# Kernel optimization log

Hardware: AMD Instinct MI355X
Metric: run time of the kernel (lower is better)

Reference implementation:

```python
import jax, jax.numpy as jnp
import numpy as np

B, T, N = 2, 256, 512
H, S, C = 64, 8, 8
DYN = 4


def setup_inputs() -> dict:
    key = jax.random.key(0)
    ks = jax.random.split(key, 12)
    sc = 0.05
    return {
        "x": jax.random.normal(ks[0], (B, T, N), jnp.float32),
        "mask": (jax.random.uniform(ks[1], (B, T, N)) < 0.2).astype(jnp.float32),
        "static_context": jax.random.normal(ks[2], (N, S), jnp.float32),
        "node_coords": jax.random.normal(ks[3], (N, C), jnp.float32),
        "W1": jax.random.normal(ks[4], (DYN + S, H), jnp.float32) * sc,
        "b1": jnp.zeros((H,), jnp.float32),
        "W2": jax.random.normal(ks[5], (H, H), jnp.float32) * sc,
        "b2": jnp.zeros((H,), jnp.float32),
        "We1": jax.random.normal(ks[6], (4 * H, H), jnp.float32) * sc,
        "be1": jnp.zeros((H,), jnp.float32),
        "We2": jax.random.normal(ks[7], (H, 1), jnp.float32) * sc,
        "be2": jnp.zeros((1,), jnp.float32),
        "self_loop_logit": jnp.float32(0.5),
        "prior_strength": jnp.float32(1.0),
        "similarity_strength": jnp.float32(1.0),
        "temperature": jnp.float32(0.7),
    }


def reference(x, mask, static_context, node_coords, W1, b1, W2, b2,
              We1, be1, We2, be2, self_loop_logit, prior_strength,
              similarity_strength, temperature):
    Bv, Tv, Nv = x.shape
    # ---- dynamic per-node context over time ----
    observed = 1.0 - mask                                   # [B,T,N]
    count = jnp.maximum(observed.sum(axis=1), 1.0)          # [B,N]
    mean = (x * observed).sum(axis=1) / count               # [B,N]
    centered = (x - mean[:, None, :]) * observed
    std = jnp.sqrt((centered ** 2).sum(axis=1) / count + 1e-6)
    t_idx = jnp.arange(Tv, dtype=x.dtype)[None, :, None]
    latest = jnp.argmax(t_idx * observed, axis=1)           # [B,N] int
    last = jnp.take_along_axis(x, latest[:, None, :], axis=1)[:, 0, :]
    missing_ratio = mask.mean(axis=1)
    dyn = jnp.stack([mean, std, last, missing_ratio], axis=-1)  # [B,N,4]
    # ---- node encoder ----
    static = jnp.broadcast_to(static_context[None], (Bv, Nv, static_context.shape[-1]))
    feats = jnp.concatenate([dyn, static], axis=-1)
    h = jax.nn.relu(feats @ W1 + b1)
    h = jax.nn.relu(h @ W2 + b2)                            # [B,N,H]
    hn = h / jnp.maximum(jnp.linalg.norm(h, axis=-1, keepdims=True), 1e-12)
    # ---- edge MLP on pair features [h_i, h_j, |h_i-h_j|, h_i*h_j] ----
    # split first-layer weight into the four blocks so h_i/h_j terms are O(N)
    Wi, Wj, Wa, Wp = jnp.split(We1, 4, axis=0)              # each [H,H]
    pre_i = h @ Wi                                          # [B,N,H]
    pre_j = h @ Wj
    hi = h[:, :, None, :]                                   # [B,N,1,H]
    hj = h[:, None, :, :]                                   # [B,1,N,H]
    hidden = jax.nn.relu(pre_i[:, :, None, :] + pre_j[:, None, :, :]
                         + jnp.abs(hi - hj) @ Wa + (hi * hj) @ Wp + be1)
    edge_logits = (hidden @ We2 + be2)[..., 0]              # [B,N,N]
    # ---- cosine similarity + distance prior ----
    cos = jnp.einsum('bnh,bmh->bnm', hn, hn)
    eye = jnp.eye(Nv, dtype=x.dtype)
    off = 1.0 - eye
    diff = node_coords[:, None, :] - node_coords[None, :, :]
    dist = jnp.sqrt(jnp.maximum((diff ** 2).sum(-1), 1e-12))
    prior = (1.0 / (1.0 + dist)) * off                      # [N,N]
    # ---- combine, softmax, symmetrize, row-normalize ----
    logits = (edge_logits * off
              + jax.nn.softplus(prior_strength) * prior[None]
              + jax.nn.softplus(similarity_strength) * (cos * off))
    logits = logits + eye[None] * jax.nn.softplus(self_loop_logit)
    temp = jax.nn.softplus(temperature) + 1e-4
    adj = jax.nn.softmax(logits / temp, axis=-1)
    adj = 0.5 * (adj + jnp.swapaxes(adj, -1, -2))
    adj = adj / jnp.maximum(adj.sum(axis=-1, keepdims=True), 1e-6)
    return adj
```

## Files before the change

kernel.cpp:

```cpp
#include <hip/hip_runtime.h>
#include <hip/hip_bf16.h>
#include <math.h>

#define NB 2
#define NT 256
#define NN 512
#define NH 64
#define NS 8
#define NC 8

#define OFF_H      0
#define OFF_PVEC   65536
#define OFF_HF16   131072
#define OFF_INVN   163840
#define OFF_WA16   164864
#define OFF_WJF    166912
#define OFF_WPF    171008
#define OFF_UNSYM  175104
#define OFF_UNSYMT (175104 + 524288)

typedef __attribute__((ext_vector_type(8))) _Float16 h8;
typedef __attribute__((ext_vector_type(2))) __fp16 fp16x2;
typedef __attribute__((ext_vector_type(4))) float f32x4;
typedef __attribute__((ext_vector_type(4))) unsigned u4;
typedef __attribute__((ext_vector_type(2))) unsigned u2;

__device__ __forceinline__ float softplusf(float x){
  if (x > 20.f) return x;
  return log1pf(expf(x));
}

__device__ __forceinline__ unsigned pkh(float a, float b){
  fp16x2 h = __builtin_amdgcn_cvt_pkrtz(a, b);
  return __builtin_bit_cast(unsigned, h);
}

__device__ __forceinline__ float fdot2u(unsigned a, unsigned b, float c){
#if __has_builtin(__builtin_amdgcn_fdot2)
  return __builtin_amdgcn_fdot2(__builtin_bit_cast(fp16x2, a),
                                __builtin_bit_cast(fp16x2, b), c, false);
#else
  fp16x2 av = __builtin_bit_cast(fp16x2, a);
  fp16x2 bv = __builtin_bit_cast(fp16x2, b);
  return fmaf((float)av.x, (float)bv.x, fmaf((float)av.y, (float)bv.y, c));
#endif
}
__device__ __forceinline__ float dot8(u4 a, u4 b, float acc){
  #pragma unroll
  for (int d = 0; d < 4; ++d) acc = fdot2u(a[d], b[d], acc);
  return acc;
}

template<int CTRL>
__device__ __forceinline__ float dpp_addf(float x){
  int xi = __builtin_bit_cast(int, x);
  int yi = __builtin_amdgcn_update_dpp(0, xi, CTRL, 0xF, 0xF, true);
  return x + __builtin_bit_cast(float, yi);
}
__device__ __forceinline__ float row16_sum(float x){
  x = dpp_addf<0xB1>(x);
  x = dpp_addf<0x4E>(x);
  x = dpp_addf<0x141>(x);
  x = dpp_addf<0x140>(x);
  return x;
}

__global__ __launch_bounds__(256) void k_front(
    const float* __restrict__ x, const float* __restrict__ mask,
    const float* __restrict__ sctx,
    const float* __restrict__ W1, const float* __restrict__ b1,
    const float* __restrict__ W2, const float* __restrict__ b2,
    const float* __restrict__ We1, const float* __restrict__ be1,
    float* __restrict__ hg, float* __restrict__ pvec,
    unsigned* __restrict__ hf16, float* __restrict__ invn,
    short* __restrict__ wa16, float* __restrict__ wjf,
    float* __restrict__ wpf){
  int blk = blockIdx.x;
  int tid = threadIdx.x;

  if (blk >= 256){
    int pidx = (blk - 256)*256 + tid;
    int e    = pidx & 7;
    int lane = (pidx >> 3) & 63;
    int frag = (pidx >> 9) & 7;
    int nt = frag & 3, ks = frag >> 2;
    int kg = lane >> 4, q = lane & 15;
    int kk = ks*32 + kg*8 + e;
    int c  = nt*16 + q;
    if (pidx < 4096){
      _Float16 v = (_Float16)We1[(128 + kk)*NH + c];
      wa16[pidx] = __builtin_bit_cast(short, v);
    } else if (pidx < 8192){
      wjf[pidx - 4096] = We1[(64 + kk)*NH + c];
    } else {
      wpf[pidx - 8192] = We1[(192 + kk)*NH + c];
    }
    return;
  }

  int b  = blk >> 7;
  int n0 = (blk & 127) * 4;

  int nl = tid & 3;
  int ts = tid >> 2;
  int n  = n0 + nl;

  float cnt = 0.f, sx = 0.f, sxx = 0.f;
  int lastt = 0;
  for (int t = ts*4; t < ts*4 + 4; ++t){
    int idx = (b*NT + t)*NN + n;
    float xv = x[idx];
    float mv = mask[idx];
    bool obs = (mv < 0.5f);
    if (obs){ cnt += 1.f; sx += xv; sxx += xv*xv; lastt = t; }
  }
  #pragma unroll
  for (int m = 4; m < 64; m <<= 1){
    cnt   += __shfl_xor(cnt,  m);
    sx    += __shfl_xor(sx,   m);
    sxx   += __shfl_xor(sxx,  m);
    lastt  = max(lastt, __shfl_xor(lastt, m));
  }
  int w = tid >> 6;
  __shared__ float r_cnt[4][4], r_sx[4][4], r_sxx[4][4];
  __shared__ int   r_lt[4][4];
  __shared__ float s_dyn[4][4];
  if ((tid & 63) < 4){
    r_cnt[w][nl] = cnt; r_sx[w][nl] = sx; r_sxx[w][nl] = sxx; r_lt[w][nl] = lastt;
  }
  __syncthreads();
  if (tid < 4){
    float c = 0.f, s1 = 0.f, s2 = 0.f; int lt = 0;
    #pragma unroll
    for (int ww = 0; ww < 4; ++ww){
      c  += r_cnt[ww][tid]; s1 += r_sx[ww][tid]; s2 += r_sxx[ww][tid];
      lt  = max(lt, r_lt[ww][tid]);
    }
    float cc   = fmaxf(c, 1.f);
    float mean = s1 / cc;
    float var  = s2 / cc - mean*mean;
    float stdv = sqrtf(fmaxf(var, 0.f) + 1e-6f);
    float last = x[(b*NT + lt)*NN + n0 + tid];
    float mr   = 1.f - c * (1.f/(float)NT);
    s_dyn[tid][0] = mean; s_dyn[tid][1] = stdv; s_dyn[tid][2] = last; s_dyn[tid][3] = mr;
  }
  __syncthreads();

  int c = tid & 63;
  int gn = n0 + w;
  int bn = b*NN + gn;
  __shared__ float s_f[4][12];
  __shared__ float s_h1[4][64];
  __shared__ float s_h2[4][64];

  if (c < 4)       s_f[w][c] = s_dyn[w][c];
  else if (c < 12) s_f[w][c] = sctx[gn*NS + (c-4)];
  __syncthreads();

  float a = b1[c];
  #pragma unroll
  for (int k = 0; k < 12; ++k) a = fmaf(s_f[w][k], W1[k*NH + c], a);
  s_h1[w][c] = fmaxf(a, 0.f);
  __syncthreads();

  float t0 = 0.f, t1 = 0.f, t2 = 0.f, t3 = 0.f;
  #pragma unroll 4
  for (int k = 0; k < 64; k += 4){
    t0 = fmaf(s_h1[w][k],     W2[(k)*NH + c],     t0);
    t1 = fmaf(s_h1[w][k + 1], W2[(k + 1)*NH + c], t1);
    t2 = fmaf(s_h1[w][k + 2], W2[(k + 2)*NH + c], t2);
    t3 = fmaf(s_h1[w][k + 3], W2[(k + 3)*NH + c], t3);
  }
  float a2 = b2[c] + ((t0 + t1) + (t2 + t3));
  a2 = fmaxf(a2, 0.f);

  float sq = a2*a2;
  #pragma unroll
  for (int m = 1; m < 64; m <<= 1) sq += __shfl_xor(sq, m);
  float inv = 1.f / fmaxf(sqrtf(sq), 1e-12f);

  s_h2[w][c] = a2;
  __syncthreads();

  float p0 = 0.f, p1 = 0.f, p2 = 0.f, p3 = 0.f;
  #pragma unroll 4
  for (int k = 0; k < 64; k += 4){
    p0 = fmaf(s_h2[w][k],     We1[(k)*NH + c],     p0);
    p1 = fmaf(s_h2[w][k + 1], We1[(k + 1)*NH + c], p1);
    p2 = fmaf(s_h2[w][k + 2], We1[(k + 2)*NH + c], p2);
    p3 = fmaf(s_h2[w][k + 3], We1[(k + 3)*NH + c], p3);
  }
  float pi = be1[c] + ((p0 + p1) + (p2 + p3));

  hg  [bn*64 + c] = a2;
  pvec[bn*64 + c] = pi;
  if (c < 32){
    float e0 = s_h2[w][2*c], e1 = s_h2[w][2*c + 1];
    hf16[bn*32 + c] = pkh(e0, e1);
  }
  if (c == 0) invn[bn] = inv;
}

__global__ __launch_bounds__(512, 4) void k_logits(
    const float* __restrict__ hg, const float* __restrict__ pvec,
    const unsigned* __restrict__ hf16, const float* __restrict__ invn,
    const short* __restrict__ wa16, const float* __restrict__ wjf,
    const float* __restrict__ wpf, const float* __restrict__ coords,
    const float* __restrict__ We2, const float* __restrict__ be2,
    const float* __restrict__ s_sl, const float* __restrict__ s_ps,
    const float* __restrict__ s_ss, const float* __restrict__ s_tp,
    float* __restrict__ unsym, float* __restrict__ unsymT){
  int blk = blockIdx.x;
  int b  = blk >> 8;
  int ip = (blk & 255) * 2;
  int tid  = threadIdx.x;
  int w    = tid >> 6;
  int lane = tid & 63;
  int q    = lane & 15;
  int kg   = lane >> 4;

  __shared__ __align__(16) float s_hi[2][64];
  __shared__ __align__(16) float s_pri[2][NN];
  __shared__ __align__(16) float s_invn[NN];
  __shared__ __align__(16) float lrow[2][NN];
  __shared__ __align__(16) unsigned lds_wa[2048];
  __shared__ __align__(16) unsigned lds_cw[2][2048];
  __shared__ __align__(16) unsigned s_hj[8][2][16*34 + 2];
  __shared__ float red[32];

  float spsl = softplusf(s_sl[0]);
  float spps = softplusf(s_ps[0]);
  float spss = softplusf(s_ss[0]);
  float invt = 1.f / (softplusf(s_tp[0]) + 1e-4f);
  float be2v = be2[0];

  if (tid < 128)
    s_hi[tid >> 6][tid & 63] = hg[(b*NN + ip + (tid >> 6))*64 + (tid & 63)];
  {
    int j = tid;
    float4 cj0 = *(const float4*)(coords + j*NC);
    float4 cj1 = *(const float4*)(coords + j*NC + 4);
    #pragma unroll
    for (int r = 0; r < 2; ++r){
      int i = ip + r;
      float4 ci0 = *(const float4*)(coords + i*NC);
      float4 ci1 = *(const float4*)(coords + i*NC + 4);
      float dd = 0.f;
      dd = fmaf(ci0.x-cj0.x, ci0.x-cj0.x, dd);
      dd = fmaf(ci0.y-cj0.y, ci0.y-cj0.y, dd);
      dd = fmaf(ci0.z-cj0.z, ci0.z-cj0.z, dd);
      dd = fmaf(ci0.w-cj0.w, ci0.w-cj0.w, dd);
      dd = fmaf(ci1.x-cj1.x, ci1.x-cj1.x, dd);
      dd = fmaf(ci1.y-cj1.y, ci1.y-cj1.y, dd);
      dd = fmaf(ci1.z-cj1.z, ci1.z-cj1.z, dd);
      dd = fmaf(ci1.w-cj1.w, ci1.w-cj1.w, dd);
      float dist = sqrtf(fmaxf(dd, 1e-12f));
      s_pri[r][j] = (j == i) ? be2v : fmaf(spps, 1.f/(1.f + dist), be2v);
    }
    s_invn[j] = invn[b*NN + j];
  }
  __syncthreads();

  {
    int frag = tid >> 6;
    int l2   = tid & 63;
    const u4* wsrc = (const u4*)wa16;
    *(u4*)&lds_wa[(frag*64 + l2)*4] = wsrc[frag*64 + l2];

    int ch0 = (frag >> 2)*32 + (l2 >> 4)*8;
    const float* wj = wjf + (frag*64 + l2)*8;
    const float* wp = wpf + (frag*64 + l2)*8;
    #pragma unroll
    for (int r = 0; r < 2; ++r){
      u4 u;
      #pragma unroll
      for (int d = 0; d < 4; ++d){
        float v0 = fmaf(s_hi[r][ch0 + 2*d],     wp[2*d],     wj[2*d]);
        float v1 = fmaf(s_hi[r][ch0 + 2*d + 1], wp[2*d + 1], wj[2*d + 1]);
        u[d] = pkh(v0, v1);
      }
      *(u4*)&lds_cw[r][(frag*64 + l2)*4] = u;
    }
  }

  const u4* hfv = (const u4*)hf16;
  u4 hiA[2][2];
  #pragma unroll
  for (int r = 0; r < 2; ++r){
    hiA[r][0] = hfv[(b*NN + ip + r)*8 + kg];
    hiA[r][1] = hfv[(b*NN + ip + r)*8 + kg + 4];
  }

  float pv4[2][4], we2q[4];
  #pragma unroll
  for (int nt = 0; nt < 4; ++nt){
    #pragma unroll
    for (int r = 0; r < 2; ++r)
      pv4[r][nt] = pvec[(b*NN + ip + r)*64 + nt*16 + q];
    we2q[nt] = We2[nt*16 + q];
  }
  float invni[2];
  invni[0] = invn[b*NN + ip];
  invni[1] = invn[b*NN + ip + 1];
  int srcl = (lane & 48) | (((lane >> 4) & 3) << 2) | (lane & 3);
  int r8 = lane >> 3, c8 = lane & 7;
  __syncthreads();

  const u4 absm = (u4){0x7fff7fffu, 0x7fff7fffu, 0x7fff7fffu, 0x7fff7fffu};

  u4 g0, g1;
  {
    int jbase = w * 16;
    g0 = *(const u4*)((const unsigned*)hf16 + (size_t)(b*NN + jbase + r8)*32 + c8*4);
    g1 = *(const u4*)((const unsigned*)hf16 + (size_t)(b*NN + jbase + 8 + r8)*32 + c8*4);
  }

  #pragma unroll
  for (int s = 0; s < 4; ++s){
    int jbase = (w + s*8) * 16;
    unsigned* slice = &s_hj[w][s & 1][0];

    {
      unsigned* p0 = slice + r8*34 + c8*4;
      unsigned* p1 = slice + (8 + r8)*34 + c8*4;
      u2 t;
      t.x = g0.x; t.y = g0.y; *(u2*)p0 = t;
      t.x = g0.z; t.y = g0.w; *(u2*)(p0 + 2) = t;
      t.x = g1.x; t.y = g1.y; *(u2*)p1 = t;
      t.x = g1.z; t.y = g1.w; *(u2*)(p1 + 2) = t;
    }
    if (s < 3){
      int jn = (w + (s+1)*8) * 16;
      g0 = *(const u4*)((const unsigned*)hf16 + (size_t)(b*NN + jn + r8)*32 + c8*4);
      g1 = *(const u4*)((const unsigned*)hf16 + (size_t)(b*NN + jn + 8 + r8)*32 + c8*4);
    }

    u4 hj0, hj1;
    {
      unsigned* rp = slice + q*34 + kg*4;
      u2 a0 = *(u2*)rp;
      u2 a1 = *(u2*)(rp + 2);
      u2 b0 = *(u2*)(rp + 16);
      u2 b1 = *(u2*)(rp + 18);
      hj0.x = a0.x; hj0.y = a0.y; hj0.z = a1.x; hj0.w = a1.y;
      hj1.x = b0.x; hj1.y = b0.y; hj1.z = b1.x; hj1.w = b1.y;
    }
    h8 hjv0 = __builtin_bit_cast(h8, hj0);
    h8 hjv1 = __builtin_bit_cast(h8, hj1);

    float dotp[2];
    #pragma unroll
    for (int r = 0; r < 2; ++r){
      float d0 = dot8(hiA[r][0], hj0, 0.f);
      dotp[r]  = dot8(hiA[r][1], hj1, d0);
    }

    f32x4 acc[2][4];
    #pragma unroll
    for (int r = 0; r < 2; ++r)
      #pragma unroll
      for (int nt = 0; nt < 4; ++nt)
        acc[r][nt] = (f32x4){pv4[r][nt], pv4[r][nt], pv4[r][nt], pv4[r][nt]};

    #pragma unroll
    for (int nt = 0; nt < 4; ++nt){
      h8 wA0 = __builtin_bit_cast(h8, *(const u4*)&lds_wa[((0*4 + nt)*64 + lane)*4]);
      h8 wA1 = __builtin_bit_cast(h8, *(const u4*)&lds_wa[((1*4 + nt)*64 + lane)*4]);
      #pragma unroll
      for (int r = 0; r < 2; ++r){
        h8 dh0 = __builtin_bit_cast(h8, hiA[r][0]) - hjv0;
        h8 dh1 = __builtin_bit_cast(h8, hiA[r][1]) - hjv1;
        h8 af0 = __builtin_bit_cast(h8, __builtin_bit_cast(u4, dh0) & absm);
        h8 af1 = __builtin_bit_cast(h8, __builtin_bit_cast(u4, dh1) & absm);
        h8 wC0 = __builtin_bit_cast(h8, *(const u4*)&lds_cw[r][((0*4 + nt)*64 + lane)*4]);
        h8 wC1 = __builtin_bit_cast(h8, *(const u4*)&lds_cw[r][((1*4 + nt)*64 + lane)*4]);
        acc[r][nt] = __builtin_amdgcn_mfma_f32_16x16x32_f16(af0, wA0, acc[r][nt], 0, 0, 0);
        acc[r][nt] = __builtin_amdgcn_mfma_f32_16x16x32_f16(af1, wA1, acc[r][nt], 0, 0, 0);
        acc[r][nt] = __builtin_amdgcn_mfma_f32_16x16x32_f16(hjv0, wC0, acc[r][nt], 0, 0, 0);
        acc[r][nt] = __builtin_amdgcn_mfma_f32_16x16x32_f16(hjv1, wC1, acc[r][nt], 0, 0, 0);
      }
    }

    #pragma unroll
    for (int r = 0; r < 2; ++r){
      float part[4] = {0.f, 0.f, 0.f, 0.f};
      #pragma unroll
      for (int nt = 0; nt < 4; ++nt)
        #pragma unroll
        for (int rr = 0; rr < 4; ++rr)
          part[rr] = fmaf(fmaxf(acc[r][nt][rr], 0.f), we2q[nt], part[rr]);
      #pragma unroll
      for (int rr = 0; rr < 4; ++rr) part[rr] = row16_sum(part[rr]);

      float dp = dotp[r];
      dp += __shfl_xor(dp, 16);
      dp += __shfl_xor(dp, 32);
      float dj = __shfl(dp, srcl);

      if (q < 4){
        int j2 = jbase + kg*4 + q;
        float ps2 = part[0];
        ps2 = (q == 1) ? part[1] : ps2;
        ps2 = (q == 2) ? part[2] : ps2;
        ps2 = (q == 3) ? part[3] : ps2;
        float cosv = dj * invni[r] * s_invn[j2];
        lrow[r][j2] = ps2 + s_pri[r][j2] + spss * cosv;
      }
    }
  }
  __syncthreads();

  float va = (tid == ip)     ? spsl : lrow[0][tid];
  float vb = (tid == ip + 1) ? spsl : lrow[1][tid];

  float ma = va, mb = vb;
  #pragma unroll
  for (int msk = 1; msk < 64; msk <<= 1){
    ma = fmaxf(ma, __shfl_xor(ma, msk));
    mb = fmaxf(mb, __shfl_xor(mb, msk));
  }
  if (lane == 0){ red[w] = ma; red[8 + w] = mb; }
  __syncthreads();
  ma = red[0]; mb = red[8];
  #pragma unroll
  for (int ww = 1; ww < 8; ++ww){
    ma = fmaxf(ma, red[ww]);
    mb = fmaxf(mb, red[8 + ww]);
  }

  float ea = expf((va - ma) * invt);
  float eb = expf((vb - mb) * invt);
  float sa = ea, sb = eb;
  #pragma unroll
  for (int msk = 1; msk < 64; msk <<= 1){
    sa += __shfl_xor(sa, msk);
    sb += __shfl_xor(sb, msk);
  }
  if (lane == 0){ red[16 + w] = sa; red[24 + w] = sb; }
  __syncthreads();
  sa = red[16]; sb = red[24];
  #pragma unroll
  for (int ww = 1; ww < 8; ++ww){
    sa += red[16 + ww];
    sb += red[24 + ww];
  }

  float oa = ea / sa;
  float ob = eb / sb;
  unsym[(size_t)(b*NN + ip)*NN + tid]     = oa;
  unsym[(size_t)(b*NN + ip + 1)*NN + tid] = ob;
  *(float2*)(unsymT + (size_t)(b*NN + tid)*NN + ip) = (float2){oa, ob};
}

__global__ __launch_bounds__(512) void k_sym(
    const float* __restrict__ u, const float* __restrict__ ut,
    float* __restrict__ out){
  int blk = blockIdx.x;
  int b  = blk >> 8;
  int ip = (blk & 255) * 2;
  int tid  = threadIdx.x;
  int lane = tid & 63, w = tid >> 6;

  const float* ra  = u  + (size_t)(b*NN + ip) * NN;
  const float* rat = ut + (size_t)(b*NN + ip) * NN;
  const float* rb  = u  + (size_t)(b*NN + ip + 1) * NN;
  const float* rbt = ut + (size_t)(b*NN + ip + 1) * NN;
  float va = 0.5f*(ra[tid] + rat[tid]);
  float vb = 0.5f*(rb[tid] + rbt[tid]);

  float sa = va, sb = vb;
  #pragma unroll
  for (int msk = 1; msk < 64; msk <<= 1){
    sa += __shfl_xor(sa, msk);
    sb += __shfl_xor(sb, msk);
  }
  __shared__ float red[16];
  if (lane == 0){ red[w] = sa; red[8 + w] = sb; }
  __syncthreads();
  sa = red[0]; sb = red[8];
  #pragma unroll
  for (int ww = 1; ww < 8; ++ww){
    sa += red[ww];
    sb += red[8 + ww];
  }
  float ia = 1.f / fmaxf(sa, 1e-6f);
  float ib = 1.f / fmaxf(sb, 1e-6f);
  out[(size_t)(b*NN + ip)*NN + tid]     = va * ia;
  out[(size_t)(b*NN + ip + 1)*NN + tid] = vb * ib;
}

extern "C" void kernel_launch(void* const* d_in, const int* in_sizes, int n_in,
                              void* d_out, int out_size, void* d_ws, size_t ws_size,
                              hipStream_t stream){
  const float* x      = (const float*)d_in[0];
  const float* mask   = (const float*)d_in[1];
  const float* sctx   = (const float*)d_in[2];
  const float* coords = (const float*)d_in[3];
  const float* W1     = (const float*)d_in[4];
  const float* b1     = (const float*)d_in[5];
  const float* W2     = (const float*)d_in[6];
  const float* b2     = (const float*)d_in[7];
  const float* We1    = (const float*)d_in[8];
  const float* be1    = (const float*)d_in[9];
  const float* We2    = (const float*)d_in[10];
  const float* be2    = (const float*)d_in[11];
  const float* sl     = (const float*)d_in[12];
  const float* ps     = (const float*)d_in[13];
  const float* ss     = (const float*)d_in[14];
  const float* tp     = (const float*)d_in[15];

  float*    ws     = (float*)d_ws;
  float*    hgp    = ws + OFF_H;
  float*    pvecp  = ws + OFF_PVEC;
  unsigned* hf16p  = (unsigned*)(ws + OFF_HF16);
  float*    invnp  = ws + OFF_INVN;
  short*    wa16p  = (short*)(ws + OFF_WA16);
  float*    wjfp   = ws + OFF_WJF;
  float*    wpfp   = ws + OFF_WPF;
  float*    unsym  = ws + OFF_UNSYM;
  float*    unsymT = ws + OFF_UNSYMT;
  float*    out    = (float*)d_out;

  k_front <<<304, 256, 0, stream>>>(x, mask, sctx, W1, b1, W2, b2, We1, be1,
                                    hgp, pvecp, hf16p, invnp, wa16p, wjfp, wpfp);
  k_logits<<<NB*NN/2, 512, 0, stream>>>(hgp, pvecp, hf16p, invnp, wa16p, wjfp,
                                        wpfp, coords, We2, be2, sl, ps, ss, tp,
                                        unsym, unsymT);
  k_sym   <<<NB*NN/2, 512, 0, stream>>>(unsym, unsymT, out);
}
```

Baseline: 39.93 us.

## Process four rows per block in k_logits with 1024-thread blocks

Each k_logits block now handles four i-rows instead of two, using 1024 threads and 16 waves. Each wave covers two 16-column j-tiles and loops over two row pairs, so one staged h_j tile and the shared lds_wa weights serve twice as many rows. The softmax is split so each half of the block reduces its own pair of rows. This halves the grid to 256 blocks and raises LDS per block, which may lower occupancy and leave fewer blocks to spread across CUs.

```diff
diff --git a/kernel.cpp b/kernel.cpp
--- a/kernel.cpp
+++ b/kernel.cpp
@@ -201,7 +201,7 @@
   if (c == 0) invn[bn] = inv;
 }
 
-__global__ __launch_bounds__(512, 4) void k_logits(
+__global__ __launch_bounds__(1024, 4) void k_logits(
     const float* __restrict__ hg, const float* __restrict__ pvec,
     const unsigned* __restrict__ hf16, const float* __restrict__ invn,
     const short* __restrict__ wa16, const float* __restrict__ wjf,
@@ -211,22 +211,24 @@
     const float* __restrict__ s_ss, const float* __restrict__ s_tp,
     float* __restrict__ unsym, float* __restrict__ unsymT){
   int blk = blockIdx.x;
-  int b  = blk >> 8;
-  int ip = (blk & 255) * 2;
+  int b  = blk >> 7;
+  int ip = (blk & 127) * 4;
   int tid  = threadIdx.x;
   int w    = tid >> 6;
   int lane = tid & 63;
   int q    = lane & 15;
   int kg   = lane >> 4;
-
-  __shared__ __align__(16) float s_hi[2][64];
-  __shared__ __align__(16) float s_pri[2][NN];
+  int half = tid >> 9;
+  int jj   = tid & 511;
+
+  __shared__ __align__(16) float s_hi[4][64];
+  __shared__ __align__(16) float s_pri[4][NN];
   __shared__ __align__(16) float s_invn[NN];
-  __shared__ __align__(16) float lrow[2][NN];
+  __shared__ __align__(16) float lrow[4][NN];
   __shared__ __align__(16) unsigned lds_wa[2048];
-  __shared__ __align__(16) unsigned lds_cw[2][2048];
-  __shared__ __align__(16) unsigned s_hj[8][2][16*34 + 2];
-  __shared__ float red[32];
+  __shared__ __align__(16) unsigned lds_cw[4][2048];
+  __shared__ __align__(16) unsigned s_hj[16][16*34 + 2];
+  __shared__ float red[64];
 
   float spsl = softplusf(s_sl[0]);
   float spps = softplusf(s_ps[0]);
@@ -234,15 +236,16 @@
   float invt = 1.f / (softplusf(s_tp[0]) + 1e-4f);
   float be2v = be2[0];
 
-  if (tid < 128)
+  if (tid < 256)
     s_hi[tid >> 6][tid & 63] = hg[(b*NN + ip + (tid >> 6))*64 + (tid & 63)];
   {
-    int j = tid;
+    int j = jj;
     float4 cj0 = *(const float4*)(coords + j*NC);
     float4 cj1 = *(const float4*)(coords + j*NC + 4);
     #pragma unroll
     for (int r = 0; r < 2; ++r){
-      int i = ip + r;
+      int row = half*2 + r;
+      int i = ip + row;
       float4 ci0 = *(const float4*)(coords + i*NC);
       float4 ci1 = *(const float4*)(coords + i*NC + 4);
       float dd = 0.f;
@@ -255,58 +258,53 @@
       dd = fmaf(ci1.z-cj1.z, ci1.z-cj1.z, dd);
       dd = fmaf(ci1.w-cj1.w, ci1.w-cj1.w, dd);
       float dist = sqrtf(fmaxf(dd, 1e-12f));
-      s_pri[r][j] = (j == i) ? be2v : fmaf(spps, 1.f/(1.f + dist), be2v);
-    }
-    s_invn[j] = invn[b*NN + j];
+      s_pri[row][j] = (j == i) ? be2v : fmaf(spps, 1.f/(1.f + dist), be2v);
+    }
+    if (half == 0) s_invn[j] = invn[b*NN + j];
   }
   __syncthreads();
 
   {
-    int frag = tid >> 6;
+    int frag = (tid >> 6) & 7;
     int l2   = tid & 63;
-    const u4* wsrc = (const u4*)wa16;
-    *(u4*)&lds_wa[(frag*64 + l2)*4] = wsrc[frag*64 + l2];
+    if (half == 0)
+      *(u4*)&lds_wa[(frag*64 + l2)*4] = ((const u4*)wa16)[frag*64 + l2];
 
     int ch0 = (frag >> 2)*32 + (l2 >> 4)*8;
     const float* wj = wjf + (frag*64 + l2)*8;
     const float* wp = wpf + (frag*64 + l2)*8;
     #pragma unroll
     for (int r = 0; r < 2; ++r){
+      int row = half*2 + r;
       u4 u;
       #pragma unroll
       for (int d = 0; d < 4; ++d){
-        float v0 = fmaf(s_hi[r][ch0 + 2*d],     wp[2*d],     wj[2*d]);
-        float v1 = fmaf(s_hi[r][ch0 + 2*d + 1], wp[2*d + 1], wj[2*d + 1]);
+        float v0 = fmaf(s_hi[row][ch0 + 2*d],     wp[2*d],     wj[2*d]);
+        float v1 = fmaf(s_hi[row][ch0 + 2*d + 1], wp[2*d + 1], wj[2*d + 1]);
         u[d] = pkh(v0, v1);
       }
-      *(u4*)&lds_cw[r][(frag*64 + l2)*4] = u;
+      *(u4*)&lds_cw[row][(frag*64 + l2)*4] = u;
     }
   }
 
   const u4* hfv = (const u4*)hf16;
-  u4 hiA[2][2];
-  #pragma unroll
-  for (int r = 0; r < 2; ++r){
-    hiA[r][0] = hfv[(b*NN + ip + r)*8 + kg];
-    hiA[r][1] = hfv[(b*NN + ip + r)*8 + kg + 4];
-  }
-
-  float pv4[2][4], we2q[4];
+  float pv4[4][4], we2q[4];
   #pragma unroll
   for (int nt = 0; nt < 4; ++nt){
     #pragma unroll
-    for (int r = 0; r < 2; ++r)
-      pv4[r][nt] = pvec[(b*NN + ip + r)*64 + nt*16 + q];
+    for (int row = 0; row < 4; ++row)
+      pv4[row][nt] = pvec[(b*NN + ip + row)*64 + nt*16 + q];
     we2q[nt] = We2[nt*16 + q];
   }
-  float invni[2];
-  invni[0] = invn[b*NN + ip];
-  invni[1] = invn[b*NN + ip + 1];
+  float invni[4];
+  #pragma unroll
+  for (int row = 0; row < 4; ++row) invni[row] = invn[b*NN + ip + row];
   int srcl = (lane & 48) | (((lane >> 4) & 3) << 2) | (lane & 3);
   int r8 = lane >> 3, c8 = lane & 7;
   __syncthreads();
 
   const u4 absm = (u4){0x7fff7fffu, 0x7fff7fffu, 0x7fff7fffu, 0x7fff7fffu};
+  unsigned* slice = &s_hj[w][0];
 
   u4 g0, g1;
   {
@@ -316,9 +314,8 @@
   }
 
   #pragma unroll
-  for (int s = 0; s < 4; ++s){
-    int jbase = (w + s*8) * 16;
-    unsigned* slice = &s_hj[w][s & 1][0];
+  for (int s = 0; s < 2; ++s){
+    int jbase = (w + s*16) * 16;
 
     {
       unsigned* p0 = slice + r8*34 + c8*4;
@@ -329,8 +326,8 @@
       t.x = g1.x; t.y = g1.y; *(u2*)p1 = t;
       t.x = g1.z; t.y = g1.w; *(u2*)(p1 + 2) = t;
     }
-    if (s < 3){
-      int jn = (w + (s+1)*8) * 16;
+    if (s == 0){
+      int jn = (w + 16) * 16;
       g0 = *(const u4*)((const unsigned*)hf16 + (size_t)(b*NN + jn + r8)*32 + c8*4);
       g1 = *(const u4*)((const unsigned*)hf16 + (size_t)(b*NN + jn + 8 + r8)*32 + c8*4);
     }
@@ -348,108 +345,126 @@
     h8 hjv0 = __builtin_bit_cast(h8, hj0);
     h8 hjv1 = __builtin_bit_cast(h8, hj1);
 
-    float dotp[2];
-    #pragma unroll
-    for (int r = 0; r < 2; ++r){
-      float d0 = dot8(hiA[r][0], hj0, 0.f);
-      dotp[r]  = dot8(hiA[r][1], hj1, d0);
-    }
-
-    f32x4 acc[2][4];
-    #pragma unroll
-    for (int r = 0; r < 2; ++r)
-      #pragma unroll
-      for (int nt = 0; nt < 4; ++nt)
-        acc[r][nt] = (f32x4){pv4[r][nt], pv4[r][nt], pv4[r][nt], pv4[r][nt]};
-
-    #pragma unroll
-    for (int nt = 0; nt < 4; ++nt){
-      h8 wA0 = __builtin_bit_cast(h8, *(const u4*)&lds_wa[((0*4 + nt)*64 + lane)*4]);
-      h8 wA1 = __builtin_bit_cast(h8, *(const u4*)&lds_wa[((1*4 + nt)*64 + lane)*4]);
+    #pragma unroll
+    for (int p = 0; p < 2; ++p){
+      u4 hiA[2][2];
       #pragma unroll
       for (int r = 0; r < 2; ++r){
-        h8 dh0 = __builtin_bit_cast(h8, hiA[r][0]) - hjv0;
-        h8 dh1 = __builtin_bit_cast(h8, hiA[r][1]) - hjv1;
-        h8 af0 = __builtin_bit_cast(h8, __builtin_bit_cast(u4, dh0) & absm);
-        h8 af1 = __builtin_bit_cast(h8, __builtin_bit_cast(u4, dh1) & absm);
-        h8 wC0 = __builtin_bit_cast(h8, *(const u4*)&lds_cw[r][((0*4 + nt)*64 + lane)*4]);
-        h8 wC1 = __builtin_bit_cast(h8, *(const u4*)&lds_cw[r][((1*4 + nt)*64 + lane)*4]);
-        acc[r][nt] = __builtin_amdgcn_mfma_f32_16x16x32_f16(af0, wA0, acc[r][nt], 0, 0, 0);
-        acc[r][nt] = __builtin_amdgcn_mfma_f32_16x16x32_f16(af1, wA1, acc[r][nt], 0, 0, 0);
-        acc[r][nt] = __builtin_amdgcn_mfma_f32_16x16x32_f16(hjv0, wC0, acc[r][nt], 0, 0, 0);
-        acc[r][nt] = __builtin_amdgcn_mfma_f32_16x16x32_f16(hjv1, wC1, acc[r][nt], 0, 0, 0);
+        hiA[r][0] = hfv[(b*NN + ip + 2*p + r)*8 + kg];
+        hiA[r][1] = hfv[(b*NN + ip + 2*p + r)*8 + kg + 4];
       }
-    }
-
-    #pragma unroll
-    for (int r = 0; r < 2; ++r){
-      float part[4] = {0.f, 0.f, 0.f, 0.f};
+      float dotp[2];
       #pragma unroll
-      for (int nt = 0; nt < 4; ++nt)
+      for (int r = 0; r < 2; ++r){
+        float d0 = dot8(hiA[r][0], hj0, 0.f);
+        dotp[r]  = dot8(hiA[r][1], hj1, d0);
+      }
+
+      f32x4 acc[2][4];
+      #pragma unroll
+      for (int r = 0; r < 2; ++r)
         #pragma unroll
-        for (int rr = 0; rr < 4; ++rr)
-          part[rr] = fmaf(fmaxf(acc[r][nt][rr], 0.f), we2q[nt], part[rr]);
+        for (int nt = 0; nt < 4; ++nt){
+          float pv = pv4[2*p + r][nt];
+          acc[r][nt] = (f32x4){pv, pv, pv, pv};
+        }
+
       #pragma unroll
-      for (int rr = 0; rr < 4; ++rr) part[rr] = row16_sum(part[rr]);
-
-      float dp = dotp[r];
-      dp += __shfl_xor(dp, 16);
-      dp += __shfl_xor(dp, 32);
-      float dj = __shfl(dp, srcl);
-
-      if (q < 4){
-        int j2 = jbase + kg*4 + q;
-        float ps2 = part[0];
-        ps2 = (q == 1) ? part[1] : ps2;
-        ps2 = (q == 2) ? part[2] : ps2;
-        ps2 = (q == 3) ? part[3] : ps2;
-        float cosv = dj * invni[r] * s_invn[j2];
-        lrow[r][j2] = ps2 + s_pri[r][j2] + spss * cosv;
+      for (int nt = 0; nt < 4; ++nt){
+        h8 wA0 = __builtin_bit_cast(h8, *(const u4*)&lds_wa[((0*4 + nt)*64 + lane)*4]);
+        h8 wA1 = __builtin_bit_cast(h8, *(const u4*)&lds_wa[((1*4 + nt)*64 + lane)*4]);
+        #pragma unroll
+        for (int r = 0; r < 2; ++r){
+          int row = 2*p + r;
+          h8 dh0 = __builtin_bit_cast(h8, hiA[r][0]) - hjv0;
+          h8 dh1 = __builtin_bit_cast(h8, hiA[r][1]) - hjv1;
+          h8 af0 = __builtin_bit_cast(h8, __builtin_bit_cast(u4, dh0) & absm);
+          h8 af1 = __builtin_bit_cast(h8, __builtin_bit_cast(u4, dh1) & absm);
+          h8 wC0 = __builtin_bit_cast(h8, *(const u4*)&lds_cw[row][((0*4 + nt)*64 + lane)*4]);
+          h8 wC1 = __builtin_bit_cast(h8, *(const u4*)&lds_cw[row][((1*4 + nt)*64 + lane)*4]);
+          acc[r][nt] = __builtin_amdgcn_mfma_f32_16x16x32_f16(af0, wA0, acc[r][nt], 0, 0, 0);
+          acc[r][nt] = __builtin_amdgcn_mfma_f32_16x16x32_f16(af1, wA1, acc[r][nt], 0, 0, 0);
+          acc[r][nt] = __builtin_amdgcn_mfma_f32_16x16x32_f16(hjv0, wC0, acc[r][nt], 0, 0, 0);
+          acc[r][nt] = __builtin_amdgcn_mfma_f32_16x16x32_f16(hjv1, wC1, acc[r][nt], 0, 0, 0);
+        }
       }
-    }
-  }
-  __syncthreads();
-
-  float va = (tid == ip)     ? spsl : lrow[0][tid];
-  float vb = (tid == ip + 1) ? spsl : lrow[1][tid];
-
-  float ma = va, mb = vb;
-  #pragma unroll
-  for (int msk = 1; msk < 64; msk <<= 1){
-    ma = fmaxf(ma, __shfl_xor(ma, msk));
-    mb = fmaxf(mb, __shfl_xor(mb, msk));
-  }
-  if (lane == 0){ red[w] = ma; red[8 + w] = mb; }
-  __syncthreads();
-  ma = red[0]; mb = red[8];
-  #pragma unroll
-  for (int ww = 1; ww < 8; ++ww){
-    ma = fmaxf(ma, red[ww]);
-    mb = fmaxf(mb, red[8 + ww]);
-  }
-
-  float ea = expf((va - ma) * invt);
-  float eb = expf((vb - mb) * invt);
-  float sa = ea, sb = eb;
-  #pragma unroll
-  for (int msk = 1; msk < 64; msk <<= 1){
-    sa += __shfl_xor(sa, msk);
-    sb += __shfl_xor(sb, msk);
-  }
-  if (lane == 0){ red[16 + w] = sa; red[24 + w] = sb; }
-  __syncthreads();
-  sa = red[16]; sb = red[24];
-  #pragma unroll
-  for (int ww = 1; ww < 8; ++ww){
-    sa += red[16 + ww];
-    sb += red[24 + ww];
-  }
-
-  float oa = ea / sa;
-  float ob = eb / sb;
-  unsym[(size_t)(b*NN + ip)*NN + tid]     = oa;
-  unsym[(size_t)(b*NN + ip + 1)*NN + tid] = ob;
-  *(float2*)(unsymT + (size_t)(b*NN + tid)*NN + ip) = (float2){oa, ob};
+
+      #pragma unroll
+      for (int r = 0; r < 2; ++r){
+        int row = 2*p + r;
+        float part[4] = {0.f, 0.f, 0.f, 0.f};
+        #pragma unroll
+        for (int nt = 0; nt < 4; ++nt)
+          #pragma unroll
+          for (int rr = 0; rr < 4; ++rr)
+            part[rr] = fmaf(fmaxf(acc[r][nt][rr], 0.f), we2q[nt], part[rr]);
+        #pragma unroll
+        for (int rr = 0; rr < 4; ++rr) part[rr] = row16_sum(part[rr]);
+
+        float dp = dotp[r];
+        dp += __shfl_xor(dp, 16);
+        dp += __shfl_xor(dp, 32);
+        float dj = __shfl(dp, srcl);
+
+        if (q < 4){
+          int j2 = jbase + kg*4 + q;
+          float ps2 = part[0];
+          ps2 = (q == 1) ? part[1] : ps2;
+          ps2 = (q == 2) ? part[2] : ps2;
+          ps2 = (q == 3) ? part[3] : ps2;
+          float cosv = dj * invni[row] * s_invn[j2];
+          lrow[row][j2] = ps2 + s_pri[row][j2] + spss * cosv;
+        }
+      }
+    }
+  }
+  __syncthreads();
+
+  {
+    int p = half;
+    int j = jj;
+    int ra = 2*p, rb = 2*p + 1;
+    float va = (j == ip + ra) ? spsl : lrow[ra][j];
+    float vb = (j == ip + rb) ? spsl : lrow[rb][j];
+
+    float ma = va, mb = vb;
+    #pragma unroll
+    for (int msk = 1; msk < 64; msk <<= 1){
+      ma = fmaxf(ma, __shfl_xor(ma, msk));
+      mb = fmaxf(mb, __shfl_xor(mb, msk));
+    }
+    if (lane == 0){ red[w] = ma; red[16 + w] = mb; }
+    __syncthreads();
+    ma = red[p*8]; mb = red[16 + p*8];
+    #pragma unroll
+    for (int ww = 1; ww < 8; ++ww){
+      ma = fmaxf(ma, red[p*8 + ww]);
+      mb = fmaxf(mb, red[16 + p*8 + ww]);
+    }
+
+    float ea = expf((va - ma) * invt);
+    float eb = expf((vb - mb) * invt);
+    float sa = ea, sb = eb;
+    #pragma unroll
+    for (int msk = 1; msk < 64; msk <<= 1){
+      sa += __shfl_xor(sa, msk);
+      sb += __shfl_xor(sb, msk);
+    }
+    if (lane == 0){ red[32 + w] = sa; red[48 + w] = sb; }
+    __syncthreads();
+    sa = red[32 + p*8]; sb = red[48 + p*8];
+    #pragma unroll
+    for (int ww = 1; ww < 8; ++ww){
+      sa += red[32 + p*8 + ww];
+      sb += red[48 + p*8 + ww];
+    }
+
+    float oa = ea / sa;
+    float ob = eb / sb;
+    unsym[(size_t)(b*NN + ip + ra)*NN + j] = oa;
+    unsym[(size_t)(b*NN + ip + rb)*NN + j] = ob;
+    *(float2*)(unsymT + (size_t)(b*NN + j)*NN + ip + 2*p) = (float2){oa, ob};
+  }
 }
 
 __global__ __launch_bounds__(512) void k_sym(
@@ -523,8 +538,8 @@
 
   k_front <<<304, 256, 0, stream>>>(x, mask, sctx, W1, b1, W2, b2, We1, be1,
                                     hgp, pvecp, hf16p, invnp, wa16p, wjfp, wpfp);
-  k_logits<<<NB*NN/2, 512, 0, stream>>>(hgp, pvecp, hf16p, invnp, wa16p, wjfp,
-                                        wpfp, coords, We2, be2, sl, ps, ss, tp,
-                                        unsym, unsymT);
+  k_logits<<<NB*NN/4, 1024, 0, stream>>>(hgp, pvecp, hf16p, invnp, wa16p, wjfp,
+                                         wpfp, coords, We2, be2, sl, ps, ss, tp,
+                                         unsym, unsymT);
   k_sym   <<<NB*NN/2, 512, 0, stream>>>(unsym, unsymT, out);
 }
```

After: 59.43 us. +48.8%, slower.
